# Kernel optimization log

Hardware: AMD Instinct MI355X
Metric: run time of the kernel (lower is better)

## Reference

```python
import jax, jax.numpy as jnp
import numpy as np

EMB_DIM = 1024
N_HEADS = 16
HEAD_DIM = EMB_DIM // N_HEADS


def setup_inputs() -> dict:
    key = jax.random.key(0)
    ks = jax.random.split(key, 6)
    B, T, C = 2, 2048, EMB_DIM
    s = 1.0 / np.sqrt(C)
    return {
        "x": jax.random.normal(ks[0], (B, T, C), dtype=jnp.float32),
        "W_query": jax.random.normal(ks[1], (C, C), dtype=jnp.float32) * s,
        "W_key": jax.random.normal(ks[2], (C, C), dtype=jnp.float32) * s,
        "W_value": jax.random.normal(ks[3], (C, C), dtype=jnp.float32) * s,
        "W_out": jax.random.normal(ks[4], (C, C), dtype=jnp.float32) * s,
        "b_out": jax.random.normal(ks[5], (C,), dtype=jnp.float32) * 0.01,
    }


def reference(x, W_query, W_key, W_value, W_out, b_out):
    # x: [B, T, C]. Linear weights stored as [in, out] (transposed torch layout).
    B, T, C = x.shape
    H, D = N_HEADS, HEAD_DIM

    def split_heads(t):  # [B,T,C] -> [B,H,T,D]
        return t.reshape(B, T, H, D).transpose(0, 2, 1, 3)

    q = split_heads(x @ W_query)
    k = split_heads(x @ W_key)
    v = split_heads(x @ W_value)

    scale = 1.0 / jnp.sqrt(jnp.asarray(D, dtype=x.dtype))
    att = jnp.einsum("bhqd,bhkd->bhqk", q, k) * scale  # [B,H,T,T]
    causal = jnp.tril(jnp.ones((T, T), dtype=bool))
    att = jnp.where(causal[None, None], att, jnp.asarray(-jnp.inf, dtype=att.dtype))
    att = jax.nn.softmax(att, axis=-1)
    # dropout is identity in eval / drop_rate=0
    y = jnp.einsum("bhqk,bhkd->bhqd", att, v)  # [B,H,T,D]
    y = y.transpose(0, 2, 1, 3).reshape(B, T, C)
    return y @ W_out + b_out
```

## Files before the change

kernel.cpp:

```cpp
#include <hip/hip_runtime.h>
#include <hip/hip_bf16.h>
#include <math.h>

#define Bsz 2
#define Tsz 2048
#define Csz 1024
#define Hsz 16
#define Dsz 64

typedef __attribute__((ext_vector_type(8))) short frag8;
typedef __attribute__((ext_vector_type(4))) float f4;
typedef __attribute__((ext_vector_type(8))) unsigned short us8;
typedef __attribute__((ext_vector_type(4))) _Float16 frag4h;
typedef __attribute__((ext_vector_type(8))) _Float16 frag8h;
typedef __attribute__((ext_vector_type(2))) _Float16 h2;

static __device__ __forceinline__ unsigned short f2bf(float f) {
  union { __hip_bfloat16 h; unsigned short u; } c;
  c.h = __float2bfloat16(f);
  return c.u;
}
static __device__ __forceinline__ unsigned short f2h(float f) {
  union { _Float16 h; unsigned short u; } c;
  c.h = (_Float16)f;
  return c.u;
}

#define GLDS16(g, l)                                                        \
  __builtin_amdgcn_global_load_lds(                                         \
      (const __attribute__((address_space(1))) void*)(g),                   \
      (__attribute__((address_space(3))) void*)(l), 16, 0, 0)

#define QSCALE 0.18033688f

__global__ __launch_bounds__(256) void cast_x(const float* __restrict__ x,
                                              unsigned short* __restrict__ xb) {
  const int i = (blockIdx.x * 256 + threadIdx.x) * 8;
  const float4 a = *(const float4*)(x + i);
  const float4 b = *(const float4*)(x + i + 4);
  us8 v;
  v[0] = f2bf(a.x); v[1] = f2bf(a.y); v[2] = f2bf(a.z); v[3] = f2bf(a.w);
  v[4] = f2bf(b.x); v[5] = f2bf(b.y); v[6] = f2bf(b.z); v[7] = f2bf(b.w);
  *(us8*)(xb + i) = v;
}

__global__ __launch_bounds__(256) void transpose_cast(
    const float* __restrict__ s0, const float* __restrict__ s1,
    const float* __restrict__ s2, const float* __restrict__ s3,
    unsigned short* __restrict__ d0, unsigned short* __restrict__ d1,
    unsigned short* __restrict__ d2, unsigned short* __restrict__ d3) {
  __shared__ float Ls[64][65];
  const int mat = blockIdx.x >> 8;
  const int tile = blockIdx.x & 255;
  const float* src = mat == 0 ? s0 : mat == 1 ? s1 : mat == 2 ? s2 : s3;
  unsigned short* dst = mat == 0 ? d0 : mat == 1 ? d1 : mat == 2 ? d2 : d3;
  const int tr0 = (tile >> 4) << 6, tc0 = (tile & 15) << 6;
  const int t = threadIdx.x;
  const int lr = t >> 4, lc = (t & 15) << 2;
#pragma unroll
  for (int j = 0; j < 4; ++j) {
    const float4 v = *(const float4*)(src + (size_t)(tr0 + lr + j * 16) * 1024 + tc0 + lc);
    Ls[lr + j * 16][lc + 0] = v.x;
    Ls[lr + j * 16][lc + 1] = v.y;
    Ls[lr + j * 16][lc + 2] = v.z;
    Ls[lr + j * 16][lc + 3] = v.w;
  }
  __syncthreads();
#pragma unroll
  for (int j = 0; j < 4; ++j) {
    ushort4 v;
    v.x = f2bf(Ls[lc + 0][lr + j * 16]);
    v.y = f2bf(Ls[lc + 1][lr + j * 16]);
    v.z = f2bf(Ls[lc + 2][lr + j * 16]);
    v.w = f2bf(Ls[lc + 3][lr + j * 16]);
    *(ushort4*)(dst + (size_t)(tc0 + lr + j * 16) * 1024 + tr0 + lc) = v;
  }
}

template <int MODE, int MT>
__global__ __launch_bounds__(256) void mm_bt(
    const unsigned short* __restrict__ A, const unsigned short* __restrict__ Bt,
    const float* __restrict__ bias, unsigned short* __restrict__ O0,
    unsigned short* __restrict__ O1, unsigned short* __restrict__ O2,
    float* __restrict__ Of) {
  __shared__ __align__(16) unsigned short As[MT * 32 * 64];
  __shared__ __align__(16) unsigned short Bs[128 * 64];
  const int K = 1024;
  const int tid = threadIdx.x;
  const int wave = tid >> 6, lane = tid & 63;
  const int quad = lane >> 4, l16 = lane & 15;
  const int wrow = (wave >> 1) * (MT * 16), wn = wave & 1;
  const int row0 = blockIdx.y * (MT * 32), col0 = blockIdx.x << 7;

  const int sr = lane >> 3, sg = lane & 7;
  const int g0 = sg ^ sr;
  const unsigned short* gA = A + (size_t)(row0 + wave * (MT * 8) + sr) * K + (g0 << 3);
  const unsigned short* gB = Bt + (size_t)(col0 + wave * 32 + sr) * K + (g0 << 3);

  f4 acc[MT][4];
#pragma unroll
  for (int i = 0; i < MT; ++i)
#pragma unroll
    for (int j = 0; j < 4; ++j) acc[i][j] = (f4){0.f, 0.f, 0.f, 0.f};

  for (int kk = 0; kk < K; kk += 64) {
    __syncthreads();
#pragma unroll
    for (int s = 0; s < MT; ++s)
      GLDS16(gA + kk + (size_t)(s * 8) * K, &As[(wave * (MT * 8) + s * 8) * 64]);
#pragma unroll
    for (int s = 0; s < 4; ++s)
      GLDS16(gB + kk + (size_t)(s * 8) * K, &Bs[(wave * 32 + s * 8) * 64]);
    __syncthreads();

#pragma unroll
    for (int ks = 0; ks < 2; ++ks) {
      frag8 af[MT], bf[4];
#pragma unroll
      for (int mt = 0; mt < MT; ++mt) {
        const int r = wrow + mt * 16 + l16;
        af[mt] = *(const frag8*)&As[r * 64 + (((ks * 4 + quad) ^ (l16 & 7)) << 3)];
      }
#pragma unroll
      for (int nt = 0; nt < 4; ++nt) {
        const int n = wn * 64 + nt * 16 + l16;
        bf[nt] = *(const frag8*)&Bs[n * 64 + (((ks * 4 + quad) ^ (l16 & 7)) << 3)];
      }
#pragma unroll
      for (int mt = 0; mt < MT; ++mt)
#pragma unroll
        for (int nt = 0; nt < 4; ++nt)
          acc[mt][nt] = __builtin_amdgcn_mfma_f32_16x16x32_bf16(af[mt], bf[nt], acc[mt][nt], 0, 0, 0);
    }
  }

  if (MODE == 0) {
    if (col0 < 2048) {
      const bool isK = (col0 >= 1024);
      unsigned short* dst = isK ? O1 : O0;
      const float sc = isK ? 1.0f : QSCALE;
#pragma unroll
      for (int mt = 0; mt < MT; ++mt)
#pragma unroll
        for (int nt = 0; nt < 4; ++nt) {
          const int m = row0 + wrow + mt * 16 + quad * 4;
          const int n = (col0 & 1023) + wn * 64 + nt * 16 + l16;
          const int b = m >> 11, h = n >> 6, d = n & 63;
#pragma unroll
          for (int r = 0; r < 4; ++r) {
            const int tk = (m + r) & (Tsz - 1);
            dst[(((size_t)b * Hsz + h) * Tsz + tk) * Dsz + d] = f2bf(acc[mt][nt][r] * sc);
          }
        }
    } else {
#pragma unroll
      for (int mt = 0; mt < MT; ++mt)
#pragma unroll
        for (int nt = 0; nt < 4; ++nt) {
          const int tok = row0 + wrow + mt * 16 + quad * 4;
          const int ch = (col0 - 2048) + wn * 64 + nt * 16 + l16;
          const int b = tok >> 11, tk = tok & (Tsz - 1);
          const int h = ch >> 6, d = ch & 63;
          const int t5 = tk & 31;
          const int pos = (tk & ~31) + ((t5 >> 4) << 2) + (((t5 >> 2) & 3) << 3) + (t5 & 3);
          ushort4 v;
          v.x = f2h(acc[mt][nt][0]); v.y = f2h(acc[mt][nt][1]);
          v.z = f2h(acc[mt][nt][2]); v.w = f2h(acc[mt][nt][3]);
          *(ushort4*)&O2[(((size_t)b * Hsz + h) * Dsz + d) * Tsz + pos] = v;
        }
    }
  } else {
#pragma unroll
    for (int mt = 0; mt < MT; ++mt)
#pragma unroll
      for (int nt = 0; nt < 4; ++nt) {
        const int m = row0 + wrow + mt * 16 + quad * 4;
        const int n = col0 + wn * 64 + nt * 16 + l16;
        const float bv = bias[n];
#pragma unroll
        for (int r = 0; r < 4; ++r)
          Of[(size_t)(m + r) * Csz + n] = acc[mt][nt][r] + bv;
      }
  }
}

__global__ __launch_bounds__(256, 3) void attn_mfma(
    const unsigned short* __restrict__ Qb,
    const unsigned short* __restrict__ Kb,
    const unsigned short* __restrict__ VTb,
    unsigned short* __restrict__ Y) {
  __shared__ __align__(16) float comb[3 * 64 * 37];

  const int tid = threadIdx.x;
  const int sp = tid >> 6, lane = tid & 63;
  const int quad = lane >> 4, l16 = lane & 15;

  const int bh = blockIdx.x & 31;
  const int j = 63 - (blockIdx.x >> 5);
  const int qb0 = j << 5;

  const unsigned short* Qh = Qb + (size_t)bh * Tsz * Dsz;
  const unsigned short* Kh = Kb + (size_t)bh * Tsz * Dsz;
  const unsigned short* Vh = VTb + (size_t)bh * Dsz * Tsz;

  frag8 qf[2][2];
#pragma unroll
  for (int m = 0; m < 2; ++m)
#pragma unroll
    for (int ks = 0; ks < 2; ++ks)
      qf[m][ks] = *(const frag8*)(Qh + (size_t)(qb0 + m * 16 + l16) * Dsz + ks * 32 + quad * 8);

  f4 o[2][4];
  float lsum[2] = {0.f, 0.f};
#pragma unroll
  for (int m = 0; m < 2; ++m)
#pragma unroll
    for (int nt = 0; nt < 4; ++nt) o[m][nt] = (f4){0.f, 0.f, 0.f, 0.f};
  const f4 zf = (f4){0.f, 0.f, 0.f, 0.f};

  const unsigned short* kl = Kh + (size_t)l16 * Dsz + quad * 8;
  const unsigned short* vl = Vh + (size_t)l16 * Tsz + quad * 8;

  auto LOADCH = [&](frag8 (&KF)[2][2], frag8h (&VF)[4], int c) {
#pragma unroll
    for (int n = 0; n < 2; ++n)
#pragma unroll
      for (int ks = 0; ks < 2; ++ks)
        KF[n][ks] = *(const frag8*)(kl + (size_t)(c * 32 + n * 16) * Dsz + ks * 32);
#pragma unroll
    for (int nt = 0; nt < 4; ++nt)
      VF[nt] = *(const frag8h*)(vl + (size_t)(nt * 16) * Tsz + (c << 5));
  };

  auto COMPUTECH = [&](frag8 (&KF)[2][2], frag8h (&VF)[4], int c) {
    f4 st[2][2];
#pragma unroll
    for (int n = 0; n < 2; ++n)
#pragma unroll
      for (int m = 0; m < 2; ++m) {
        f4 a = __builtin_amdgcn_mfma_f32_16x16x32_bf16(KF[n][0], qf[m][0], zf, 0, 0, 0);
        st[n][m] = __builtin_amdgcn_mfma_f32_16x16x32_bf16(KF[n][1], qf[m][1], a, 0, 0, 0);
      }
    const bool dm = (c == j);
    frag4h paf[2][2];
#pragma unroll
    for (int m = 0; m < 2; ++m) {
      const int qq = m * 16 + l16;
#pragma unroll
      for (int n = 0; n < 2; ++n) {
        const int key0 = n * 16 + quad * 4;
        float p[4];
#pragma unroll
        for (int r = 0; r < 4; ++r) {
          float sv = st[n][m][r];
          if (dm && (key0 + r > qq)) sv = -INFINITY;
          p[r] = __builtin_amdgcn_exp2f(sv);
        }
        lsum[m] += (p[0] + p[1]) + (p[2] + p[3]);
        const h2 lo = __builtin_bit_cast(h2, __builtin_amdgcn_cvt_pkrtz(p[0], p[1]));
        const h2 hi = __builtin_bit_cast(h2, __builtin_amdgcn_cvt_pkrtz(p[2], p[3]));
        paf[m][n] = __builtin_shufflevector(lo, hi, 0, 1, 2, 3);
      }
    }
#pragma unroll
    for (int m = 0; m < 2; ++m)
#pragma unroll
      for (int nt = 0; nt < 4; ++nt) {
        const frag4h vlo = __builtin_shufflevector(VF[nt], VF[nt], 0, 1, 2, 3);
        const frag4h vhi = __builtin_shufflevector(VF[nt], VF[nt], 4, 5, 6, 7);
        f4 a = __builtin_amdgcn_mfma_f32_16x16x16f16(paf[m][0], vlo, o[m][nt], 0, 0, 0);
        o[m][nt] = __builtin_amdgcn_mfma_f32_16x16x16f16(paf[m][1], vhi, a, 0, 0, 0);
      }
  };

  frag8 kfA[2][2], kfB[2][2];
  frag8h vfA[4], vfB[4];
  const int nc = (j >= sp) ? ((j - sp) >> 2) + 1 : 0;
  int c = sp, i = 0;
  if (nc > 0) LOADCH(kfA, vfA, c);
  while (i < nc) {
    if (i + 1 < nc) LOADCH(kfB, vfB, c + 4);
    COMPUTECH(kfA, vfA, c);
    ++i; c += 4;
    if (i >= nc) break;
    if (i + 1 < nc) LOADCH(kfA, vfA, c + 4);
    COMPUTECH(kfB, vfB, c);
    ++i; c += 4;
  }

  float* cp = comb + (size_t)((sp - 1) * 64 + lane) * 37;
  if (sp != 0) {
#pragma unroll
    for (int m = 0; m < 2; ++m)
#pragma unroll
      for (int nt = 0; nt < 4; ++nt)
        *(f4*)(cp + m * 16 + nt * 4) = o[m][nt];
    cp[32] = lsum[0]; cp[33] = lsum[1];
  }
  __syncthreads();
  if (sp == 0) {
#pragma unroll
    for (int s = 0; s < 3; ++s) {
      const float* rp = comb + (size_t)(s * 64 + lane) * 37;
#pragma unroll
      for (int m = 0; m < 2; ++m)
#pragma unroll
        for (int nt = 0; nt < 4; ++nt)
          o[m][nt] += *(const f4*)(rp + m * 16 + nt * 4);
      lsum[0] += rp[32]; lsum[1] += rp[33];
    }

#pragma unroll
    for (int m = 0; m < 2; ++m) {
      lsum[m] += __shfl_xor(lsum[m], 16);
      lsum[m] += __shfl_xor(lsum[m], 32);
    }
    const int b = bh >> 4, h = bh & 15;
#pragma unroll
    for (int m = 0; m < 2; ++m)
#pragma unroll
      for (int r = 0; r < 4; ++r) {
        const float inv = 1.f / __shfl(lsum[m], quad * 4 + r);
        const int tk = qb0 + m * 16 + quad * 4 + r;
        unsigned short* yp = Y + ((size_t)b * Tsz + tk) * Csz + h * 64 + l16;
#pragma unroll
        for (int nt = 0; nt < 4; ++nt)
          yp[nt * 16] = f2bf(o[m][nt][r] * inv);
      }
  }
}

extern "C" void kernel_launch(void* const* d_in, const int* in_sizes, int n_in,
                              void* d_out, int out_size, void* d_ws, size_t ws_size,
                              hipStream_t stream) {
  const float* x  = (const float*)d_in[0];
  const float* Wq = (const float*)d_in[1];
  const float* Wk = (const float*)d_in[2];
  const float* Wv = (const float*)d_in[3];
  const float* Wo = (const float*)d_in[4];
  const float* bo = (const float*)d_in[5];

  const size_t NEL = (size_t)Bsz * Tsz * Csz;
  const size_t WSZ = (size_t)Csz * Csz;
  unsigned short* xb  = (unsigned short*)d_ws;
  unsigned short* WT  = xb + NEL;
  unsigned short* WoT = WT + 3 * WSZ;
  unsigned short* Qb  = WoT + WSZ;
  unsigned short* Kb  = Qb + NEL;
  unsigned short* VTb = Kb + NEL;
  unsigned short* Yb  = VTb + NEL;

  cast_x<<<NEL / 2048, 256, 0, stream>>>(x, xb);
  transpose_cast<<<1024, 256, 0, stream>>>(Wq, Wk, Wv, Wo,
                                           WT, WT + WSZ, WT + 2 * WSZ, WoT);

  mm_bt<0, 4><<<dim3(24, 32), 256, 0, stream>>>(xb, WT, nullptr, Qb, Kb, VTb, nullptr);

  attn_mfma<<<2048, 256, 0, stream>>>(Qb, Kb, VTb, Yb);

  mm_bt<2, 2><<<dim3(8, 64), 256, 0, stream>>>(Yb, WoT, bo, nullptr, nullptr, nullptr,
                                               (float*)d_out);
}
```

Measured before the change: 206.4 us.

## Pair causal query tiles per block to balance attention work

Each attention block now processes two query tiles, a long one (63-pr) and a short one (pr), so every block does roughly equal causal work, and the grid is halved to 1024 blocks. The double-buffered K/V loop is also restructured to drop per-iteration conditionals by clamping the prefetch index. This aims to remove tail imbalance from heavy diagonal tiles. It adds a second __syncthreads per tile, serializes the two tiles within a block, and runs a redundant prefetch load on the last iteration.

```diff
diff --git a/kernel.cpp b/kernel.cpp
--- a/kernel.cpp
+++ b/kernel.cpp
@@ -196,138 +196,151 @@
   const int quad = lane >> 4, l16 = lane & 15;
 
   const int bh = blockIdx.x & 31;
-  const int j = 63 - (blockIdx.x >> 5);
-  const int qb0 = j << 5;
+  const int pr = blockIdx.x >> 5;
 
   const unsigned short* Qh = Qb + (size_t)bh * Tsz * Dsz;
   const unsigned short* Kh = Kb + (size_t)bh * Tsz * Dsz;
   const unsigned short* Vh = VTb + (size_t)bh * Dsz * Tsz;
-
-  frag8 qf[2][2];
-#pragma unroll
-  for (int m = 0; m < 2; ++m)
-#pragma unroll
-    for (int ks = 0; ks < 2; ++ks)
-      qf[m][ks] = *(const frag8*)(Qh + (size_t)(qb0 + m * 16 + l16) * Dsz + ks * 32 + quad * 8);
-
-  f4 o[2][4];
-  float lsum[2] = {0.f, 0.f};
-#pragma unroll
-  for (int m = 0; m < 2; ++m)
-#pragma unroll
-    for (int nt = 0; nt < 4; ++nt) o[m][nt] = (f4){0.f, 0.f, 0.f, 0.f};
-  const f4 zf = (f4){0.f, 0.f, 0.f, 0.f};
+  const int b = bh >> 4, h = bh & 15;
 
   const unsigned short* kl = Kh + (size_t)l16 * Dsz + quad * 8;
   const unsigned short* vl = Vh + (size_t)l16 * Tsz + quad * 8;
-
-  auto LOADCH = [&](frag8 (&KF)[2][2], frag8h (&VF)[4], int c) {
-#pragma unroll
-    for (int n = 0; n < 2; ++n)
+  const f4 zf = (f4){0.f, 0.f, 0.f, 0.f};
+
+  auto process_tile = [&](const int j) {
+    const int qb0 = j << 5;
+
+    frag8 qf[2][2];
+#pragma unroll
+    for (int m = 0; m < 2; ++m)
 #pragma unroll
       for (int ks = 0; ks < 2; ++ks)
-        KF[n][ks] = *(const frag8*)(kl + (size_t)(c * 32 + n * 16) * Dsz + ks * 32);
-#pragma unroll
-    for (int nt = 0; nt < 4; ++nt)
-      VF[nt] = *(const frag8h*)(vl + (size_t)(nt * 16) * Tsz + (c << 5));
+        qf[m][ks] = *(const frag8*)(Qh + (size_t)(qb0 + m * 16 + l16) * Dsz + ks * 32 + quad * 8);
+
+    f4 o[2][4];
+    float lsum[2] = {0.f, 0.f};
+#pragma unroll
+    for (int m = 0; m < 2; ++m)
+#pragma unroll
+      for (int nt = 0; nt < 4; ++nt) o[m][nt] = (f4){0.f, 0.f, 0.f, 0.f};
+
+    auto LOADCH = [&](frag8 (&KF)[2][2], frag8h (&VF)[4], int c) {
+#pragma unroll
+      for (int n = 0; n < 2; ++n)
+#pragma unroll
+        for (int ks = 0; ks < 2; ++ks)
+          KF[n][ks] = *(const frag8*)(kl + (size_t)(c * 32 + n * 16) * Dsz + ks * 32);
+#pragma unroll
+      for (int nt = 0; nt < 4; ++nt)
+        VF[nt] = *(const frag8h*)(vl + (size_t)(nt * 16) * Tsz + (c << 5));
+    };
+
+    auto COMPUTECH = [&](frag8 (&KF)[2][2], frag8h (&VF)[4], int c) {
+      f4 st[2][2];
+#pragma unroll
+      for (int n = 0; n < 2; ++n)
+#pragma unroll
+        for (int m = 0; m < 2; ++m) {
+          f4 a = __builtin_amdgcn_mfma_f32_16x16x32_bf16(KF[n][0], qf[m][0], zf, 0, 0, 0);
+          st[n][m] = __builtin_amdgcn_mfma_f32_16x16x32_bf16(KF[n][1], qf[m][1], a, 0, 0, 0);
+        }
+      const bool dm = (c == j);
+      frag4h paf[2][2];
+#pragma unroll
+      for (int m = 0; m < 2; ++m) {
+        const int qq = m * 16 + l16;
+#pragma unroll
+        for (int n = 0; n < 2; ++n) {
+          const int key0 = n * 16 + quad * 4;
+          float p[4];
+#pragma unroll
+          for (int r = 0; r < 4; ++r) {
+            float sv = st[n][m][r];
+            if (dm && (key0 + r > qq)) sv = -INFINITY;
+            p[r] = __builtin_amdgcn_exp2f(sv);
+          }
+          lsum[m] += (p[0] + p[1]) + (p[2] + p[3]);
+          const h2 lo = __builtin_bit_cast(h2, __builtin_amdgcn_cvt_pkrtz(p[0], p[1]));
+          const h2 hi = __builtin_bit_cast(h2, __builtin_amdgcn_cvt_pkrtz(p[2], p[3]));
+          paf[m][n] = __builtin_shufflevector(lo, hi, 0, 1, 2, 3);
+        }
+      }
+#pragma unroll
+      for (int m = 0; m < 2; ++m)
+#pragma unroll
+        for (int nt = 0; nt < 4; ++nt) {
+          const frag4h vlo = __builtin_shufflevector(VF[nt], VF[nt], 0, 1, 2, 3);
+          const frag4h vhi = __builtin_shufflevector(VF[nt], VF[nt], 4, 5, 6, 7);
+          f4 a = __builtin_amdgcn_mfma_f32_16x16x16f16(paf[m][0], vlo, o[m][nt], 0, 0, 0);
+          o[m][nt] = __builtin_amdgcn_mfma_f32_16x16x16f16(paf[m][1], vhi, a, 0, 0, 0);
+        }
+    };
+
+    frag8 kfA[2][2], kfB[2][2];
+    frag8h vfA[4], vfB[4];
+    const int nc = (j >= sp) ? ((j - sp) >> 2) + 1 : 0;
+    if (nc > 0) {
+      const int clast = sp + ((nc - 1) << 2);
+      int c = sp;
+      int rem = nc;
+      LOADCH(kfA, vfA, c);
+      while (rem >= 2) {
+        const int c1 = c + 4;
+        const int c2 = (c + 8 <= clast) ? (c + 8) : clast;
+        LOADCH(kfB, vfB, c1);
+        COMPUTECH(kfA, vfA, c);
+        LOADCH(kfA, vfA, c2);
+        COMPUTECH(kfB, vfB, c1);
+        rem -= 2;
+        c += 8;
+      }
+      if (rem) COMPUTECH(kfA, vfA, c);
+    }
+
+    float* cp = comb + (size_t)((sp - 1) * 64 + lane) * 37;
+    if (sp != 0) {
+#pragma unroll
+      for (int m = 0; m < 2; ++m)
+#pragma unroll
+        for (int nt = 0; nt < 4; ++nt)
+          *(f4*)(cp + m * 16 + nt * 4) = o[m][nt];
+      cp[32] = lsum[0]; cp[33] = lsum[1];
+    }
+    __syncthreads();
+    if (sp == 0) {
+#pragma unroll
+      for (int s = 0; s < 3; ++s) {
+        const float* rp = comb + (size_t)(s * 64 + lane) * 37;
+#pragma unroll
+        for (int m = 0; m < 2; ++m)
+#pragma unroll
+          for (int nt = 0; nt < 4; ++nt)
+            o[m][nt] += *(const f4*)(rp + m * 16 + nt * 4);
+        lsum[0] += rp[32]; lsum[1] += rp[33];
+      }
+
+#pragma unroll
+      for (int m = 0; m < 2; ++m) {
+        lsum[m] += __shfl_xor(lsum[m], 16);
+        lsum[m] += __shfl_xor(lsum[m], 32);
+      }
+#pragma unroll
+      for (int m = 0; m < 2; ++m)
+#pragma unroll
+        for (int r = 0; r < 4; ++r) {
+          const float inv = 1.f / __shfl(lsum[m], quad * 4 + r);
+          const int tk = qb0 + m * 16 + quad * 4 + r;
+          unsigned short* yp = Y + ((size_t)b * Tsz + tk) * Csz + h * 64 + l16;
+#pragma unroll
+          for (int nt = 0; nt < 4; ++nt)
+            yp[nt * 16] = f2bf(o[m][nt][r] * inv);
+        }
+    }
+    __syncthreads();
   };
 
-  auto COMPUTECH = [&](frag8 (&KF)[2][2], frag8h (&VF)[4], int c) {
-    f4 st[2][2];
-#pragma unroll
-    for (int n = 0; n < 2; ++n)
-#pragma unroll
-      for (int m = 0; m < 2; ++m) {
-        f4 a = __builtin_amdgcn_mfma_f32_16x16x32_bf16(KF[n][0], qf[m][0], zf, 0, 0, 0);
-        st[n][m] = __builtin_amdgcn_mfma_f32_16x16x32_bf16(KF[n][1], qf[m][1], a, 0, 0, 0);
-      }
-    const bool dm = (c == j);
-    frag4h paf[2][2];
-#pragma unroll
-    for (int m = 0; m < 2; ++m) {
-      const int qq = m * 16 + l16;
-#pragma unroll
-      for (int n = 0; n < 2; ++n) {
-        const int key0 = n * 16 + quad * 4;
-        float p[4];
-#pragma unroll
-        for (int r = 0; r < 4; ++r) {
-          float sv = st[n][m][r];
-          if (dm && (key0 + r > qq)) sv = -INFINITY;
-          p[r] = __builtin_amdgcn_exp2f(sv);
-        }
-        lsum[m] += (p[0] + p[1]) + (p[2] + p[3]);
-        const h2 lo = __builtin_bit_cast(h2, __builtin_amdgcn_cvt_pkrtz(p[0], p[1]));
-        const h2 hi = __builtin_bit_cast(h2, __builtin_amdgcn_cvt_pkrtz(p[2], p[3]));
-        paf[m][n] = __builtin_shufflevector(lo, hi, 0, 1, 2, 3);
-      }
-    }
-#pragma unroll
-    for (int m = 0; m < 2; ++m)
-#pragma unroll
-      for (int nt = 0; nt < 4; ++nt) {
-        const frag4h vlo = __builtin_shufflevector(VF[nt], VF[nt], 0, 1, 2, 3);
-        const frag4h vhi = __builtin_shufflevector(VF[nt], VF[nt], 4, 5, 6, 7);
-        f4 a = __builtin_amdgcn_mfma_f32_16x16x16f16(paf[m][0], vlo, o[m][nt], 0, 0, 0);
-        o[m][nt] = __builtin_amdgcn_mfma_f32_16x16x16f16(paf[m][1], vhi, a, 0, 0, 0);
-      }
-  };
-
-  frag8 kfA[2][2], kfB[2][2];
-  frag8h vfA[4], vfB[4];
-  const int nc = (j >= sp) ? ((j - sp) >> 2) + 1 : 0;
-  int c = sp, i = 0;
-  if (nc > 0) LOADCH(kfA, vfA, c);
-  while (i < nc) {
-    if (i + 1 < nc) LOADCH(kfB, vfB, c + 4);
-    COMPUTECH(kfA, vfA, c);
-    ++i; c += 4;
-    if (i >= nc) break;
-    if (i + 1 < nc) LOADCH(kfA, vfA, c + 4);
-    COMPUTECH(kfB, vfB, c);
-    ++i; c += 4;
-  }
-
-  float* cp = comb + (size_t)((sp - 1) * 64 + lane) * 37;
-  if (sp != 0) {
-#pragma unroll
-    for (int m = 0; m < 2; ++m)
-#pragma unroll
-      for (int nt = 0; nt < 4; ++nt)
-        *(f4*)(cp + m * 16 + nt * 4) = o[m][nt];
-    cp[32] = lsum[0]; cp[33] = lsum[1];
-  }
-  __syncthreads();
-  if (sp == 0) {
-#pragma unroll
-    for (int s = 0; s < 3; ++s) {
-      const float* rp = comb + (size_t)(s * 64 + lane) * 37;
-#pragma unroll
-      for (int m = 0; m < 2; ++m)
-#pragma unroll
-        for (int nt = 0; nt < 4; ++nt)
-          o[m][nt] += *(const f4*)(rp + m * 16 + nt * 4);
-      lsum[0] += rp[32]; lsum[1] += rp[33];
-    }
-
-#pragma unroll
-    for (int m = 0; m < 2; ++m) {
-      lsum[m] += __shfl_xor(lsum[m], 16);
-      lsum[m] += __shfl_xor(lsum[m], 32);
-    }
-    const int b = bh >> 4, h = bh & 15;
-#pragma unroll
-    for (int m = 0; m < 2; ++m)
-#pragma unroll
-      for (int r = 0; r < 4; ++r) {
-        const float inv = 1.f / __shfl(lsum[m], quad * 4 + r);
-        const int tk = qb0 + m * 16 + quad * 4 + r;
-        unsigned short* yp = Y + ((size_t)b * Tsz + tk) * Csz + h * 64 + l16;
-#pragma unroll
-        for (int nt = 0; nt < 4; ++nt)
-          yp[nt * 16] = f2bf(o[m][nt][r] * inv);
-      }
-  }
+  process_tile(63 - pr);
+  process_tile(pr);
 }
 
 extern "C" void kernel_launch(void* const* d_in, const int* in_sizes, int n_in,
@@ -356,7 +369,7 @@
 
   mm_bt<0, 4><<<dim3(24, 32), 256, 0, stream>>>(xb, WT, nullptr, Qb, Kb, VTb, nullptr);
 
-  attn_mfma<<<2048, 256, 0, stream>>>(Qb, Kb, VTb, Yb);
+  attn_mfma<<<1024, 256, 0, stream>>>(Qb, Kb, VTb, Yb);
 
   mm_bt<2, 2><<<dim3(8, 64), 256, 0, stream>>>(Yb, WoT, bo, nullptr, nullptr, nullptr,
                                                (float*)d_out);
```

Measured after the change: 211.9 us. 1.03x slower.
